# Performance work log

Measured on AMD Instinct MI355X. Metric: run time of the kernel, lower is better.

## Reference

```python
import jax, jax.numpy as jnp
import numpy as np

B, T_TREES, LEAVES = 1024, 34, 16
E = 128            # entity = logic = theorem embedding size
N_NF, N_LF = 4, 3  # binary numerical / logic function experts
V_ENT, V_TH = 2000, 32
GT_MAX, ENT_MAX, TH_MAX = 8, 16, 8


def setup_inputs() -> dict:
    key = jax.random.key(0)
    ks = jax.random.split(key, 24)
    s2e = 1.0 / np.sqrt(2 * E)
    s4e = 1.0 / np.sqrt(4 * E)
    se = 1.0 / np.sqrt(E)
    inp = {
        'leaf_idx': jax.random.randint(ks[0], (B, T_TREES, LEAVES), 0, V_ENT),
        'nf_ids':   jax.random.randint(ks[1], (B, T_TREES, 15), 0, N_NF),
        'lf_ids':   jax.random.randint(ks[2], (B, GT_MAX + 1), 0, N_LF),
        'th_idx':   jax.random.randint(ks[3], (B, TH_MAX), 0, V_TH),
        'ent_emb':  jax.random.normal(ks[4], (V_ENT, E)) * 0.02,
        'th_emb':   jax.random.normal(ks[5], (V_TH, E)) * 0.02,
        # nf two2one expert MLPs: Linear(2E,2E) -> ReLU -> Linear(2E,E)
        'nf_W1': jax.random.normal(ks[6], (N_NF, 2 * E, 2 * E)) * s2e,
        'nf_b1': jnp.zeros((N_NF, 2 * E)),
        'nf_W2': jax.random.normal(ks[7], (N_NF, 2 * E, E)) * s2e,
        'nf_b2': jnp.zeros((N_NF, E)),
        # lf two2one expert MLPs: Linear(2E,4E) -> ReLU -> Linear(4E,E)
        'lf_W1': jax.random.normal(ks[8], (N_LF, 2 * E, 4 * E)) * s2e,
        'lf_b1': jnp.zeros((N_LF, 4 * E)),
        'lf_W2': jax.random.normal(ks[9], (N_LF, 4 * E, E)) * s4e,
        'lf_b2': jnp.zeros((N_LF, E)),
        # higher attention linears: logic_size -> {entity,entity,theorem} size
        'he_W': jax.random.normal(ks[10], (E, E)) * se, 'he_b': jnp.zeros((E,)),
        'hg_W': jax.random.normal(ks[11], (E, E)) * se, 'hg_b': jnp.zeros((E,)),
        'ht_W': jax.random.normal(ks[12], (E, E)) * se, 'ht_b': jnp.zeros((E,)),
    }
    return inp


def _expert_mlp(x, ids, W1, b1, W2, b2):
    # x: [..., Din], ids: [...] selecting among K experts; masked sum over K (small fixed loop)
    out = jnp.zeros(x.shape[:-1] + (W2.shape[-1],), x.dtype)
    for k in range(W1.shape[0]):
        h = jax.nn.relu(x @ W1[k] + b1[k]) @ W2[k] + b2[k]
        out = out + jnp.where((ids == k)[..., None], h, 0.0)
    return out


def _attend(keys, q):
    # keys: [B, N, D], q: [B, D] -> attentive context [B, D]
    a = jax.nn.softmax(jnp.einsum('bnd,bd->bn', keys, q), axis=-1)
    return jnp.einsum('bn,bnd->bd', a, keys)


def _forward(leaf_idx, nf_ids, lf_ids, th_idx, ent_emb, th_emb,
             nf_W1, nf_b1, nf_W2, nf_b2, lf_W1, lf_b1, lf_W2, lf_b2,
             he_W, he_b, hg_W, hg_b, ht_W, ht_b):
    # leaf entity embedding lookup: [B, 34, 16, E]
    cur = ent_emb[leaf_idx]
    # recursive tree reduction over 4 levels of binary nf MLPs (batched over all nodes)
    off = 0
    for lvl in range(4):
        n = LEAVES >> (lvl + 1)  # nodes at this level: 8,4,2,1
        x = cur.reshape(cur.shape[0], T_TREES, n, 2 * E)  # concat(left,right)
        ids = nf_ids[..., off:off + n]
        off += n
        cur = _expert_mlp(x, ids, nf_W1, nf_b1, nf_W2, nf_b2)
    roots = cur[..., 0, :]                       # [B, 34, E]
    ent = roots[:, :ENT_MAX]                     # [B, 16, E] standalone entities
    pairs = roots[:, ENT_MAX:].reshape(roots.shape[0], GT_MAX + 1, 2 * E)
    stmt = _expert_mlp(pairs, lf_ids, lf_W1, lf_b1, lf_W2, lf_b2)  # [B, 9, E]
    gt = stmt[:, :GT_MAX]                        # [B, 8, E] ground truths
    obj = stmt[:, GT_MAX]                        # [B, E]    objective
    th = th_emb[th_idx]                          # [B, 8, E] theorems
    ent_ctx = _attend(ent, obj @ he_W + he_b)
    gt_ctx = _attend(gt, obj @ hg_W + hg_b)
    th_ctx = _attend(th, obj @ ht_W + ht_b)
    # higher attentive state: 2*L + E + T = 512
    return jnp.concatenate([obj, gt_ctx, ent_ctx, th_ctx], axis=-1)


def reference(leaf_idx, nf_ids, lf_ids, th_idx, ent_emb, th_emb,
              nf_W1, nf_b1, nf_W2, nf_b2, lf_W1, lf_b1, lf_W2, lf_b2,
              he_W, he_b, hg_W, hg_b, ht_W, ht_b):
    return _forward(leaf_idx, nf_ids, lf_ids, th_idx, ent_emb, th_emb,
                    nf_W1, nf_b1, nf_W2, nf_b2, lf_W1, lf_b1, lf_W2, lf_b2,
                    he_W, he_b, hg_W, hg_b, ht_W, ht_b)
```

## Files before the change

### kernel.cpp

```cpp
#include <hip/hip_runtime.h>
#include <math.h>


typedef unsigned short u16;
typedef unsigned int   u32;
typedef unsigned long long u64;
typedef __attribute__((ext_vector_type(8))) short v8s;
typedef __attribute__((ext_vector_type(4))) float f32x4;

__device__ __forceinline__ float b2f(u16 u) { return __uint_as_float(((u32)u) << 16); }
__device__ __forceinline__ u16 f2b(float f) {
  f = (f == f) ? f : 0.f;
  u32 x = __float_as_uint(f);
  u32 r = x + 0x7fffu + ((x >> 16) & 1u);
  return (u16)(r >> 16);
}

__device__ __forceinline__ void g2lds16(const void* g, void* l) {
  __builtin_amdgcn_global_load_lds(
      (const __attribute__((address_space(1))) void*)g,
      (__attribute__((address_space(3))) void*)l, 16, 0, 0);
}

#define NTREE 34816
#define RLEAF 9216


__global__ __launch_bounds__(256) void perm_hist_k(
    const int* __restrict__ nf, int* __restrict__ bh,
    const int CB, const int bt0, const int nb)
{
  const int gid = blockIdx.x * 256 + threadIdx.x;
  int id = -1, lr = 0, cofs = 12, ioff = 14, shift = 0;
  if (gid < 8 * CB)       { lr = gid;          cofs = 0;  ioff = 0;  shift = 3; }
  else if (gid < 12 * CB) { lr = gid - 8*CB;   cofs = 4;  ioff = 8;  shift = 2; }
  else if (gid < 14 * CB) { lr = gid - 12*CB;  cofs = 8;  ioff = 12; shift = 1; }
  else if (gid < 15 * CB) { lr = gid - 14*CB;          }
  if (gid < 15 * CB) {
    int bt = bt0 + (lr >> shift);
    int n  = lr & ((1 << shift) - 1);
    id = nf[bt * 15 + ioff + n];
  }
  __shared__ int lcnt[16];
  if (threadIdx.x < 16) lcnt[threadIdx.x] = 0;
  __syncthreads();
  const int lane = threadIdx.x & 63;
  #pragma unroll
  for (int e = 0; e < 4; ++e) {
    u64 m = __ballot(id == e);
    if (m && lane == __builtin_ctzll(m))
      atomicAdd(&lcnt[cofs + e], (int)__popcll(m));
  }
  __syncthreads();
  if (threadIdx.x < 16)
    bh[threadIdx.x * nb + blockIdx.x] = lcnt[threadIdx.x];
}

__global__ __launch_bounds__(1024) void perm_scan_k(
    int* __restrict__ bh, int* __restrict__ cnt, const int nb)
{
  const int s = threadIdx.x >> 6;
  const int lane = threadIdx.x & 63;
  int carry = 0;
  for (int b0 = 0; b0 < nb; b0 += 64) {
    const int b = b0 + lane;
    int v = (b < nb) ? bh[s * nb + b] : 0;
    int x = v;
    #pragma unroll
    for (int d = 1; d < 64; d <<= 1) {
      int y = __shfl_up(x, d);
      if (lane >= d) x += y;
    }
    if (b < nb) bh[s * nb + b] = carry + x - v;
    carry += __shfl(x, 63);
  }
  if (lane == 0) cnt[s] = carry;
}

__global__ __launch_bounds__(256) void perm_scatter_k(
    const int* __restrict__ nf, const int* __restrict__ bh,
    int* __restrict__ perm, const int CB, const int bt0, const int nb)
{
  const int gid = blockIdx.x * 256 + threadIdx.x;
  int id = -1, lr = 0, rows = CB, cofs = 12, pofs = 56 * CB, ioff = 14, shift = 0;
  if (gid < 8 * CB)       { lr = gid;          rows = 8*CB; cofs = 0;  pofs = 0;      ioff = 0;  shift = 3; }
  else if (gid < 12 * CB) { lr = gid - 8*CB;   rows = 4*CB; cofs = 4;  pofs = 32*CB;  ioff = 8;  shift = 2; }
  else if (gid < 14 * CB) { lr = gid - 12*CB;  rows = 2*CB; cofs = 8;  pofs = 48*CB;  ioff = 12; shift = 1; }
  else if (gid < 15 * CB) { lr = gid - 14*CB;                 }
  if (gid < 15 * CB) {
    int bt = bt0 + (lr >> shift);
    int n  = lr & ((1 << shift) - 1);
    id = nf[bt * 15 + ioff + n];
  }
  __shared__ int wc[4][16];
  const int w = threadIdx.x >> 6, lane = threadIdx.x & 63;
  if (lane < 16) wc[w][lane] = 0;
  __syncthreads();
  u64 msave[4];
  #pragma unroll
  for (int e = 0; e < 4; ++e) {
    u64 m = __ballot(id == e);
    msave[e] = m;
    if (m && lane == __builtin_ctzll(m))
      wc[w][cofs + e] = (int)__popcll(m);
  }
  __syncthreads();
  #pragma unroll
  for (int e = 0; e < 4; ++e) {
    if (id == e) {
      const int slot = cofs + e;
      int base = bh[slot * nb + blockIdx.x];
      #pragma unroll
      for (int w2 = 0; w2 < 3; ++w2)
        if (w2 < w) base += wc[w2][slot];
      perm[pofs + e * rows + base +
           (int)__popcll(msave[e] & ((1ull << lane) - 1ull))] = lr;
    }
  }
}

__global__ __launch_bounds__(256) void leaf_perm_k(
    const int* __restrict__ lf, int* __restrict__ cnt, int* __restrict__ perm)
{
  const int gid = blockIdx.x * 256 + threadIdx.x;
  const int id = lf[gid];
  const int lane = threadIdx.x & 63;
  for (int e = 0; e < 3; ++e) {
    u64 m = __ballot(id == e);
    if (!m) continue;
    int leader = __builtin_ctzll(m);
    int bp = 0;
    if (lane == leader) bp = atomicAdd(&cnt[e], (int)__popcll(m));
    bp = __shfl(bp, leader);
    if (id == e)
      perm[e * RLEAF + bp + (int)__popcll(m & ((1ull << lane) - 1ull))] = gid;
  }
}

__global__ __launch_bounds__(256) void transpose_k(
    const float* __restrict__ s0, const float* __restrict__ s1,
    const float* __restrict__ s2, const float* __restrict__ s3,
    const float* __restrict__ s4,
    u16* __restrict__ d0, u16* __restrict__ d1, u16* __restrict__ d2,
    u16* __restrict__ d3, u16* __restrict__ d4)
{
  __shared__ float tile[16][17];
  const int t = threadIdx.x;
  const int idx0 = blockIdx.x * 256;
  if (idx0 < 983040) {
    const float* s; u16* d; int tb, estr, O, kt, mt, e;
    int tloc0;
    if (idx0 < 262144)      { s = s0; d = d0; tb = 0;      estr = 65536;  O = 256; }
    else if (idx0 < 393216) { s = s1; d = d1; tb = 262144; estr = 32768;  O = 128; }
    else if (idx0 < 786432) { s = s2; d = d2; tb = 393216; estr = 131072; O = 512; }
    else                    { s = s3; d = d3; tb = 786432; estr = 65536;  O = 128; }
    tloc0 = idx0 - tb;
    const int blk = tloc0 >> 9;
    const int hb  = (tloc0 >> 8) & 1;
    if (idx0 < 262144)      { kt = blk & 7;  mt = (blk >> 3) & 15; e = blk >> 7; }
    else if (idx0 < 393216) { kt = blk & 7;  mt = (blk >> 3) & 7;  e = blk >> 6; }
    else if (idx0 < 786432) { kt = blk & 7;  mt = (blk >> 3) & 31; e = blk >> 8; }
    else                    { kt = blk & 15; mt = (blk >> 4) & 7;  e = blk >> 7; }
    const int o0 = mt * 16;
    const int k0 = kt * 32 + hb * 16;
    tile[t >> 4][t & 15] = s[(size_t)e * estr + (size_t)(k0 + (t >> 4)) * O + o0 + (t & 15)];
    __syncthreads();
    d[tloc0 + t] = f2b(tile[((t >> 7) << 3) + (t & 7)][(t >> 3) & 15]);
  } else {
    int tl = idx0 + t - 983040;
    d4[tl] = f2b(s4[tl]);
  }
}

template<int HID, int NEXP, int MODE, int MR>
__global__ __launch_bounds__(256, 2) void mlp_k(
    const u16* __restrict__ src, const int* __restrict__ lidx,
    const u16* __restrict__ emb,
    const int* __restrict__ perm, const int* __restrict__ cnt,
    const int rows, const int bt0,
    const u16* __restrict__ W1f, const float* __restrict__ b1,
    const u16* __restrict__ W2f, const float* __restrict__ b2,
    u16* __restrict__ dst)
{
  constexpr int NT  = MR / 16;
  constexpr int MT1 = HID / 64;
  constexpr int K2  = HID / 32;
  constexpr int PD1 = (MT1 <= 4) ? 2 : 1;
  constexpr int NB1 = PD1 + 1;
  constexpr int XB  = MR * 512;
  constexpr int HB  = MR * HID * 2;
  constexpr int UB  = XB > HB ? XB : HB;
  __shared__ __align__(16) char uni[UB];
  __shared__ int rid[MR], soff[2 * MR];
  u16* const xs = (u16*)uni;
  u16* const hs = (u16*)uni;

  int bin = -1, tile = 0, cb = 0;
  {
    int rem = blockIdx.x;
    #pragma unroll
    for (int e = 0; e < NEXP; ++e) {
      int ce = cnt[e];
      int tt = (ce + MR - 1) / MR;
      if (bin < 0) {
        if (rem < tt) { bin = e; tile = rem; cb = ce; }
        else rem -= tt;
      }
    }
  }
  if (bin < 0) return;
  const int rbase = tile * MR;
  const int tid = threadIdx.x;
  const int w  = tid >> 6;
  const int lane = tid & 63;
  const int lm = lane & 15;
  const int lq = lane >> 4;

  const u16* const W1b = W1f + ((size_t)(bin * (HID / 16) + w * MT1) << 12) + lane * 8;
  const u16* const W2b = W2f + ((size_t)((bin * 8 + w * 2) * K2) << 9) + lane * 8;

  v8s afb[NB1][MT1];
  #pragma unroll
  for (int d = 0; d < PD1; ++d)
    #pragma unroll
    for (int m = 0; m < MT1; ++m)
      afb[d][m] = *(const v8s*)(W1b + (size_t)(m * 8 + d) * 512);

  if (tid < MR) {
    int rl = rbase + tid;
    int rlc = rl < cb ? rl : (cb - 1);
    rlc = rlc < 0 ? 0 : rlc;
    int rc = perm[(size_t)bin * rows + rlc];
    rc = rc < 0 ? 0 : (rc >= rows ? rows - 1 : rc);
    rid[tid] = (rl < cb) ? rc : -1;
    if (MODE == 0) {
      int bt = bt0 + (rc >> 3), node = rc & 7;
      int ia = lidx[bt * 16 + node * 2];
      int ib = lidx[bt * 16 + node * 2 + 1];
      ia = ia < 0 ? 0 : (ia > 1999 ? 1999 : ia);
      ib = ib < 0 ? 0 : (ib > 1999 ? 1999 : ib);
      soff[2 * tid]     = ia * 256;
      soff[2 * tid + 1] = ib * 256;
    } else {
      int base;
      if (MODE == 1) base = rc * 512;
      else { int bq = rc / 9, g = rc - bq * 9; base = (bq * 34 + 16 + 2 * g) * 256; }
      soff[2 * tid]     = base;
      soff[2 * tid + 1] = base + 256;
    }
  }
  __syncthreads();

  const char* const sb = (MODE == 0) ? (const char*)emb : (const char*)src;
  #pragma unroll
  for (int i = 0; i < MR / 8; ++i) {
    int d = i * 256 + tid;
    int r = d >> 5, c32d = d & 31;
    int cS = c32d ^ ((r & 7) << 1);
    const char* ga = sb + (size_t)(u32)soff[2 * r + (cS >> 4)] + (cS & 15) * 16;
    char* la = uni + ((size_t)(i * 256 + (tid & 192)) << 4);
    g2lds16(ga, la);
  }
  __syncthreads();

  int rdn[NT];
  #pragma unroll
  for (int n = 0; n < NT; ++n) rdn[n] = rid[n * 16 + lm];

  f32x4 acc[MT1][NT];
  #pragma unroll
  for (int m = 0; m < MT1; ++m)
    #pragma unroll
    for (int n = 0; n < NT; ++n)
      acc[m][n] = f32x4{0.f, 0.f, 0.f, 0.f};

  v8s bfr2[2][NT];
  #pragma unroll
  for (int n = 0; n < NT; ++n) {
    int r = n * 16 + lm;
    int cs = lq ^ ((lm & 7) << 1);
    bfr2[0][n] = *(const v8s*)(xs + r * 256 + cs * 8);
  }
  #pragma unroll
  for (int k = 0; k < 8; ++k) {
    const int cur = k % NB1;
    if (k + PD1 < 8) {
      const int nx = (k + PD1) % NB1;
      #pragma unroll
      for (int m = 0; m < MT1; ++m)
        afb[nx][m] = *(const v8s*)(W1b + (size_t)(m * 8 + k + PD1) * 512);
    }
    const int cb_ = k & 1;
    if (k < 7) {
      #pragma unroll
      for (int n = 0; n < NT; ++n) {
        int r = n * 16 + lm;
        int cs = ((k + 1) * 4 + lq) ^ ((lm & 7) << 1);
        bfr2[cb_ ^ 1][n] = *(const v8s*)(xs + r * 256 + cs * 8);
      }
    }
    __builtin_amdgcn_s_setprio(1);
    #pragma unroll
    for (int m = 0; m < MT1; ++m)
      #pragma unroll
      for (int n = 0; n < NT; ++n)
        acc[m][n] = __builtin_amdgcn_mfma_f32_16x16x32_bf16(afb[cur][m], bfr2[cb_][n], acc[m][n], 0, 0, 0);
    __builtin_amdgcn_s_setprio(0);
  }

  v8s afb2[3][2];
  #pragma unroll
  for (int m = 0; m < 2; ++m)
    afb2[0][m] = *(const v8s*)(W2b + (size_t)(m * K2) * 512);
  #pragma unroll
  for (int m = 0; m < 2; ++m)
    afb2[1][m] = *(const v8s*)(W2b + (size_t)(m * K2 + 1) * 512);

  __syncthreads();

  const float* b1b = b1 + bin * HID;
  #pragma unroll
  for (int m = 0; m < MT1; ++m) {
    const int f = (w * MT1 + m) * 16 + lq * 4;
    float bb0 = b1b[f], bb1 = b1b[f + 1], bb2 = b1b[f + 2], bb3 = b1b[f + 3];
    #pragma unroll
    for (int n = 0; n < NT; ++n) {
      union { u16 h[4]; uint2 v; } pk;
      f32x4 a = acc[m][n];
      pk.h[0] = f2b(fmaxf(a.x + bb0, 0.f));
      pk.h[1] = f2b(fmaxf(a.y + bb1, 0.f));
      pk.h[2] = f2b(fmaxf(a.z + bb2, 0.f));
      pk.h[3] = f2b(fmaxf(a.w + bb3, 0.f));
      int r = n * 16 + lm;
      int cs = (f >> 3) ^ ((lm & 7) << 1);
      *(uint2*)(uni + (size_t)r * (HID * 2) + (cs << 4) + (f & 7) * 2) = pk.v;
    }
  }
  __syncthreads();

  f32x4 acc2[2][NT];
  #pragma unroll
  for (int m = 0; m < 2; ++m)
    #pragma unroll
    for (int n = 0; n < NT; ++n)
      acc2[m][n] = f32x4{0.f, 0.f, 0.f, 0.f};

  #pragma unroll
  for (int n = 0; n < NT; ++n) {
    int r = n * 16 + lm;
    int cs = lq ^ ((lm & 7) << 1);
    bfr2[0][n] = *(const v8s*)(hs + (size_t)r * HID + cs * 8);
  }
  #pragma unroll
  for (int k = 0; k < K2; ++k) {
    const int cur = k % 3;
    if (k < K2 - 2) {
      const int nx2 = (k + 2) % 3;
      #pragma unroll
      for (int m = 0; m < 2; ++m)
        afb2[nx2][m] = *(const v8s*)(W2b + (size_t)(m * K2 + k + 2) * 512);
    }
    const int cb_ = k & 1;
    if (k < K2 - 1) {
      #pragma unroll
      for (int n = 0; n < NT; ++n) {
        int r = n * 16 + lm;
        int cs = ((k + 1) * 4 + lq) ^ ((lm & 7) << 1);
        bfr2[cb_ ^ 1][n] = *(const v8s*)(hs + (size_t)r * HID + cs * 8);
      }
    }
    __builtin_amdgcn_s_setprio(1);
    #pragma unroll
    for (int m = 0; m < 2; ++m)
      #pragma unroll
      for (int n = 0; n < NT; ++n)
        acc2[m][n] = __builtin_amdgcn_mfma_f32_16x16x32_bf16(afb2[cur][m], bfr2[cb_][n], acc2[m][n], 0, 0, 0);
    __builtin_amdgcn_s_setprio(0);
  }

  __syncthreads();
  const float* b2b = b2 + bin * 128;
  #pragma unroll
  for (int m = 0; m < 2; ++m) {
    const int f = (w * 2 + m) * 16 + lq * 4;
    float bb0 = b2b[f], bb1 = b2b[f + 1], bb2 = b2b[f + 2], bb3 = b2b[f + 3];
    #pragma unroll
    for (int n = 0; n < NT; ++n) {
      union { u16 h[4]; uint2 v; } pk;
      f32x4 a = acc2[m][n];
      pk.h[0] = f2b(a.x + bb0);
      pk.h[1] = f2b(a.y + bb1);
      pk.h[2] = f2b(a.z + bb2);
      pk.h[3] = f2b(a.w + bb3);
      int r = n * 16 + lm;
      int c = (w * 2 + m) * 2 + (lq >> 1);
      int cs = c ^ ((lm & 7) << 1);
      *(uint2*)(uni + r * 256 + cs * 16 + (lq & 1) * 8) = pk.v;
    }
  }
  __syncthreads();
  #pragma unroll
  for (int i = 0; i < MR / 16; ++i) {
    int cg = i * 256 + tid;
    int r = cg >> 4, sub = cg & 15;
    int rg = rid[r];
    if (rg >= 0) {
      uint4 v = *(const uint4*)(uni + r * 256 + ((sub ^ ((r & 7) << 1)) << 4));
      *(uint4*)((char*)dst + (size_t)rg * 256 + sub * 16) = v;
    }
  }
}

__global__ __launch_bounds__(128) void attn_k(
    const u16* __restrict__ stmt, const u16* __restrict__ roots,
    const float* __restrict__ themb, const int* __restrict__ thidx,
    const float* __restrict__ wHe, const float* __restrict__ bHe,
    const float* __restrict__ wHg, const float* __restrict__ bHg,
    const float* __restrict__ wHt, const float* __restrict__ bHt,
    float* __restrict__ out)
{
  const int b = blockIdx.x, t = threadIdx.x;
  __shared__ float obj_s[128], q_s[128], keys_s[16 * 132], a_s[16];

  const float obj = b2f(stmt[((size_t)b * 9 + 8) * 128 + t]);
  obj_s[t] = obj;
  out[(size_t)b * 512 + t] = obj;
  __syncthreads();

  for (int a = 0; a < 3; ++a) {
    int cntk;
    const float *Wt, *bv;
    if (a == 0) {
      cntk = 8; Wt = wHg; bv = bHg;
      for (int j = 0; j < 8; ++j)
        keys_s[j * 132 + t] = b2f(stmt[((size_t)b * 9 + j) * 128 + t]);
    } else if (a == 1) {
      cntk = 16; Wt = wHe; bv = bHe;
      for (int j = 0; j < 16; ++j)
        keys_s[j * 132 + t] = b2f(roots[((size_t)b * 34 + j) * 128 + t]);
    } else {
      cntk = 8; Wt = wHt; bv = bHt;
      for (int j = 0; j < 8; ++j) {
        int ti = thidx[b * 8 + j] & 31;
        keys_s[j * 132 + t] = themb[(size_t)ti * 128 + t];
      }
    }
    float qa = bv[t];
    for (int k = 0; k < 128; ++k) qa += obj_s[k] * Wt[k * 128 + t];
    q_s[t] = (qa == qa) ? qa : 0.f;
    __syncthreads();
    {
      int j = t >> 3, s = t & 7;
      if (j < cntk) {
        float sc = 0.f;
        #pragma unroll
        for (int k = 0; k < 16; ++k)
          sc += keys_s[j * 132 + s * 16 + k] * q_s[s * 16 + k];
        sc += __shfl_xor(sc, 1);
        sc += __shfl_xor(sc, 2);
        sc += __shfl_xor(sc, 4);
        if (s == 0) a_s[j] = (sc == sc) ? sc : 0.f;
      }
    }
    __syncthreads();
    if (t < 16) {
      float v = (t < cntk) ? a_s[t] : -3.0e38f;
      float mx = v;
      #pragma unroll
      for (int d = 1; d < 16; d <<= 1) mx = fmaxf(mx, __shfl_xor(mx, d));
      float e = (t < cntk) ? expf(v - mx) : 0.f;
      float sm = e;
      #pragma unroll
      for (int d = 1; d < 16; d <<= 1) sm += __shfl_xor(sm, d);
      if (t < cntk) a_s[t] = e / sm;
    }
    __syncthreads();
    float c = 0.f;
    for (int j = 0; j < cntk; ++j) c += a_s[j] * keys_s[j * 132 + t];
    out[(size_t)b * 512 + 128 * (a + 1) + t] = c;
    __syncthreads();
  }
}

extern "C" void kernel_launch(void* const* d_in, const int* in_sizes, int n_in,
                              void* d_out, int out_size, void* d_ws, size_t ws_size,
                              hipStream_t stream)
{
  const int*   leaf_idx = (const int*)d_in[0];
  const int*   nf_ids   = (const int*)d_in[1];
  const int*   lf_ids   = (const int*)d_in[2];
  const int*   th_idx   = (const int*)d_in[3];
  const float* ent_emb  = (const float*)d_in[4];
  const float* th_emb   = (const float*)d_in[5];
  const float* nf_W1 = (const float*)d_in[6];
  const float* nf_b1 = (const float*)d_in[7];
  const float* nf_W2 = (const float*)d_in[8];
  const float* nf_b2 = (const float*)d_in[9];
  const float* lf_W1 = (const float*)d_in[10];
  const float* lf_b1 = (const float*)d_in[11];
  const float* lf_W2 = (const float*)d_in[12];
  const float* lf_b2 = (const float*)d_in[13];
  const float* he_W = (const float*)d_in[14];
  const float* he_b = (const float*)d_in[15];
  const float* hg_W = (const float*)d_in[16];
  const float* hg_b = (const float*)d_in[17];
  const float* ht_W = (const float*)d_in[18];
  const float* ht_b = (const float*)d_in[19];

  int CB = NTREE;
  while (CB > 544 && 14500000ull + (unsigned long long)CB * 3320ull > (unsigned long long)ws_size)
    CB >>= 1;
  const int nch = NTREE / CB;
  const int NB = (15 * CB + 255) / 256;

  char* ws = (char*)d_ws;
  size_t off = 0;
  auto take = [&](size_t bytes) -> char* {
    char* p = ws + off;
    off = (off + bytes + 255) & ~(size_t)255;
    return p;
  };
  int* cnt      = (int*)take(8192);
  int* leafperm = (int*)take((size_t)3 * RLEAF * 4);
  int* chperm   = (int*)take((size_t)60 * CB * 4);
  int* bh       = (int*)take((size_t)16 * NB * 4);
  u16* wN1  = (u16*)take((size_t)4 * 256 * 256 * 2);
  u16* wN2  = (u16*)take((size_t)4 * 128 * 256 * 2);
  u16* wL1  = (u16*)take((size_t)3 * 512 * 256 * 2);
  u16* wL2  = (u16*)take((size_t)3 * 128 * 512 * 2);
  u16* embB = (u16*)take((size_t)2000 * 128 * 2);
  u16* bufA  = (u16*)take((size_t)CB * 8 * 128 * 2);
  u16* bufB  = (u16*)take((size_t)CB * 4 * 128 * 2);
  u16* roots = (u16*)take((size_t)NTREE * 128 * 2);
  u16* stmt  = (u16*)take((size_t)RLEAF * 128 * 2);

  int* leafcnt = cnt + nch * 16;

  hipMemsetAsync(cnt, 0, (size_t)(nch * 16 + 8) * 4, stream);
  transpose_k<<<4840, 256, 0, stream>>>(nf_W1, nf_W2, lf_W1, lf_W2, ent_emb,
                                        wN1, wN2, wL1, wL2, embB);
  leaf_perm_k<<<36, 256, 0, stream>>>(lf_ids, leafcnt, leafperm);

  for (int c = 0; c < nch; ++c) {
    const int bt0 = c * CB;
    int* ccnt = cnt + c * 16;
    perm_hist_k<<<NB, 256, 0, stream>>>(nf_ids, bh, CB, bt0, NB);
    perm_scan_k<<<1, 1024, 0, stream>>>(bh, ccnt, NB);
    perm_scatter_k<<<NB, 256, 0, stream>>>(nf_ids, bh, chperm, CB, bt0, NB);
    mlp_k<256, 4, 0, 96><<<(8 * CB + 95) / 96 + 4, 256, 0, stream>>>(
        nullptr, leaf_idx, embB, chperm, ccnt, 8 * CB, bt0,
        wN1, nf_b1, wN2, nf_b2, bufA);
    mlp_k<256, 4, 1, 96><<<(4 * CB + 95) / 96 + 4, 256, 0, stream>>>(
        bufA, nullptr, nullptr, chperm + 32 * CB, ccnt + 4, 4 * CB, 0,
        wN1, nf_b1, wN2, nf_b2, bufB);
    mlp_k<256, 4, 1, 64><<<(2 * CB + 63) / 64 + 4, 256, 0, stream>>>(
        bufB, nullptr, nullptr, chperm + 48 * CB, ccnt + 8, 2 * CB, 0,
        wN1, nf_b1, wN2, nf_b2, bufA);
    mlp_k<256, 4, 1, 64><<<(CB + 63) / 64 + 4, 256, 0, stream>>>(
        bufA, nullptr, nullptr, chperm + 56 * CB, ccnt + 12, CB, 0,
        wN1, nf_b1, wN2, nf_b2, roots + (size_t)bt0 * 128);
  }

  mlp_k<512, 3, 2, 32><<<RLEAF / 32 + 3, 256, 0, stream>>>(
      roots, nullptr, nullptr, leafperm, leafcnt, RLEAF, 0,
      wL1, lf_b1, wL2, lf_b2, stmt);

  attn_k<<<1024, 128, 0, stream>>>(stmt, roots, th_emb, th_idx,
                                   he_W, he_b, hg_W, hg_b, ht_W, ht_b,
                                   (float*)d_out);
}
```

Baseline: 292.7 us.

## Merge setup kernels and hoist per-chunk histograms into one launch

Folds the weight transpose/bf16 conversion, the leaf expert permutation and the per-chunk numeric-function histograms into a single setup kernel. The per-chunk scans then run as one multi-block launch, so fewer small kernels are launched and the chunk loop now only holds the scatter and MLP kernels. The histogram buffer is sized per chunk and the workspace budget estimate is raised a little to match. Separately, the attention query projection is unrolled with four partial accumulators to shorten the dependent FMA chain.

```diff
diff --git a/kernel.cpp b/kernel.cpp
--- a/kernel.cpp
+++ b/kernel.cpp
@@ -25,56 +25,113 @@
 #define NTREE 34816
 #define RLEAF 9216
 
-
-__global__ __launch_bounds__(256) void perm_hist_k(
+__global__ __launch_bounds__(256) void setup_k(
+    const float* __restrict__ s0, const float* __restrict__ s1,
+    const float* __restrict__ s2, const float* __restrict__ s3,
+    const float* __restrict__ s4,
+    u16* __restrict__ d0, u16* __restrict__ d1, u16* __restrict__ d2,
+    u16* __restrict__ d3, u16* __restrict__ d4,
+    const int* __restrict__ lf, int* __restrict__ leafcnt, int* __restrict__ leafperm,
     const int* __restrict__ nf, int* __restrict__ bh,
-    const int CB, const int bt0, const int nb)
+    const int CB, const int NB)
 {
-  const int gid = blockIdx.x * 256 + threadIdx.x;
-  int id = -1, lr = 0, cofs = 12, ioff = 14, shift = 0;
-  if (gid < 8 * CB)       { lr = gid;          cofs = 0;  ioff = 0;  shift = 3; }
-  else if (gid < 12 * CB) { lr = gid - 8*CB;   cofs = 4;  ioff = 8;  shift = 2; }
-  else if (gid < 14 * CB) { lr = gid - 12*CB;  cofs = 8;  ioff = 12; shift = 1; }
-  else if (gid < 15 * CB) { lr = gid - 14*CB;          }
-  if (gid < 15 * CB) {
-    int bt = bt0 + (lr >> shift);
-    int n  = lr & ((1 << shift) - 1);
-    id = nf[bt * 15 + ioff + n];
-  }
+  __shared__ float tile[16][17];
   __shared__ int lcnt[16];
-  if (threadIdx.x < 16) lcnt[threadIdx.x] = 0;
-  __syncthreads();
-  const int lane = threadIdx.x & 63;
-  #pragma unroll
-  for (int e = 0; e < 4; ++e) {
-    u64 m = __ballot(id == e);
-    if (m && lane == __builtin_ctzll(m))
-      atomicAdd(&lcnt[cofs + e], (int)__popcll(m));
-  }
-  __syncthreads();
-  if (threadIdx.x < 16)
-    bh[threadIdx.x * nb + blockIdx.x] = lcnt[threadIdx.x];
+  const int t = threadIdx.x;
+  const int bid = blockIdx.x;
+
+  if (bid < 4840) {
+    const int idx0 = bid * 256;
+    if (idx0 < 983040) {
+      const float* s; u16* d; int tb, estr, O, kt, mt, e;
+      int tloc0;
+      if (idx0 < 262144)      { s = s0; d = d0; tb = 0;      estr = 65536;  O = 256; }
+      else if (idx0 < 393216) { s = s1; d = d1; tb = 262144; estr = 32768;  O = 128; }
+      else if (idx0 < 786432) { s = s2; d = d2; tb = 393216; estr = 131072; O = 512; }
+      else                    { s = s3; d = d3; tb = 786432; estr = 65536;  O = 128; }
+      tloc0 = idx0 - tb;
+      const int blk = tloc0 >> 9;
+      const int hb  = (tloc0 >> 8) & 1;
+      if (idx0 < 262144)      { kt = blk & 7;  mt = (blk >> 3) & 15; e = blk >> 7; }
+      else if (idx0 < 393216) { kt = blk & 7;  mt = (blk >> 3) & 7;  e = blk >> 6; }
+      else if (idx0 < 786432) { kt = blk & 7;  mt = (blk >> 3) & 31; e = blk >> 8; }
+      else                    { kt = blk & 15; mt = (blk >> 4) & 7;  e = blk >> 7; }
+      const int o0 = mt * 16;
+      const int k0 = kt * 32 + hb * 16;
+      tile[t >> 4][t & 15] = s[(size_t)e * estr + (size_t)(k0 + (t >> 4)) * O + o0 + (t & 15)];
+      __syncthreads();
+      d[tloc0 + t] = f2b(tile[((t >> 7) << 3) + (t & 7)][(t >> 3) & 15]);
+    } else {
+      int tl = idx0 + t - 983040;
+      d4[tl] = f2b(s4[tl]);
+    }
+  } else if (bid < 4876) {
+    const int gid = (bid - 4840) * 256 + t;
+    const int id = lf[gid];
+    const int lane = t & 63;
+    for (int e = 0; e < 3; ++e) {
+      u64 m = __ballot(id == e);
+      if (!m) continue;
+      int leader = __builtin_ctzll(m);
+      int bp = 0;
+      if (lane == leader) bp = atomicAdd(&leafcnt[e], (int)__popcll(m));
+      bp = __shfl(bp, leader);
+      if (id == e)
+        leafperm[e * RLEAF + bp + (int)__popcll(m & ((1ull << lane) - 1ull))] = gid;
+    }
+  } else {
+    const int hb2 = bid - 4876;
+    const int c = hb2 / NB, b = hb2 - c * NB;
+    const int bt0 = c * CB;
+    int* bhc = bh + (size_t)c * 16 * NB;
+    const int gid = b * 256 + t;
+    int id = -1, lr = 0, cofs = 12, ioff = 14, shift = 0;
+    if (gid < 8 * CB)       { lr = gid;          cofs = 0;  ioff = 0;  shift = 3; }
+    else if (gid < 12 * CB) { lr = gid - 8*CB;   cofs = 4;  ioff = 8;  shift = 2; }
+    else if (gid < 14 * CB) { lr = gid - 12*CB;  cofs = 8;  ioff = 12; shift = 1; }
+    else if (gid < 15 * CB) { lr = gid - 14*CB;  }
+    if (gid < 15 * CB) {
+      int bt = bt0 + (lr >> shift);
+      int n  = lr & ((1 << shift) - 1);
+      id = nf[bt * 15 + ioff + n];
+    }
+    if (t < 16) lcnt[t] = 0;
+    __syncthreads();
+    const int lane = t & 63;
+    #pragma unroll
+    for (int e = 0; e < 4; ++e) {
+      u64 m = __ballot(id == e);
+      if (m && lane == __builtin_ctzll(m))
+        atomicAdd(&lcnt[cofs + e], (int)__popcll(m));
+    }
+    __syncthreads();
+    if (t < 16)
+      bhc[t * NB + b] = lcnt[t];
+  }
 }
 
 __global__ __launch_bounds__(1024) void perm_scan_k(
     int* __restrict__ bh, int* __restrict__ cnt, const int nb)
 {
+  const int c = blockIdx.x;
+  int* bhc = bh + (size_t)c * 16 * nb;
+  int* cntc = cnt + c * 16;
   const int s = threadIdx.x >> 6;
   const int lane = threadIdx.x & 63;
   int carry = 0;
   for (int b0 = 0; b0 < nb; b0 += 64) {
     const int b = b0 + lane;
-    int v = (b < nb) ? bh[s * nb + b] : 0;
+    int v = (b < nb) ? bhc[s * nb + b] : 0;
     int x = v;
     #pragma unroll
     for (int d = 1; d < 64; d <<= 1) {
       int y = __shfl_up(x, d);
       if (lane >= d) x += y;
     }
-    if (b < nb) bh[s * nb + b] = carry + x - v;
+    if (b < nb) bhc[s * nb + b] = carry + x - v;
     carry += __shfl(x, 63);
   }
-  if (lane == 0) cnt[s] = carry;
+  if (lane == 0) cntc[s] = carry;
 }
 
 __global__ __launch_bounds__(256) void perm_scatter_k(
@@ -116,59 +173,6 @@
       perm[pofs + e * rows + base +
            (int)__popcll(msave[e] & ((1ull << lane) - 1ull))] = lr;
     }
-  }
-}
-
-__global__ __launch_bounds__(256) void leaf_perm_k(
-    const int* __restrict__ lf, int* __restrict__ cnt, int* __restrict__ perm)
-{
-  const int gid = blockIdx.x * 256 + threadIdx.x;
-  const int id = lf[gid];
-  const int lane = threadIdx.x & 63;
-  for (int e = 0; e < 3; ++e) {
-    u64 m = __ballot(id == e);
-    if (!m) continue;
-    int leader = __builtin_ctzll(m);
-    int bp = 0;
-    if (lane == leader) bp = atomicAdd(&cnt[e], (int)__popcll(m));
-    bp = __shfl(bp, leader);
-    if (id == e)
-      perm[e * RLEAF + bp + (int)__popcll(m & ((1ull << lane) - 1ull))] = gid;
-  }
-}
-
-__global__ __launch_bounds__(256) void transpose_k(
-    const float* __restrict__ s0, const float* __restrict__ s1,
-    const float* __restrict__ s2, const float* __restrict__ s3,
-    const float* __restrict__ s4,
-    u16* __restrict__ d0, u16* __restrict__ d1, u16* __restrict__ d2,
-    u16* __restrict__ d3, u16* __restrict__ d4)
-{
-  __shared__ float tile[16][17];
-  const int t = threadIdx.x;
-  const int idx0 = blockIdx.x * 256;
-  if (idx0 < 983040) {
-    const float* s; u16* d; int tb, estr, O, kt, mt, e;
-    int tloc0;
-    if (idx0 < 262144)      { s = s0; d = d0; tb = 0;      estr = 65536;  O = 256; }
-    else if (idx0 < 393216) { s = s1; d = d1; tb = 262144; estr = 32768;  O = 128; }
-    else if (idx0 < 786432) { s = s2; d = d2; tb = 393216; estr = 131072; O = 512; }
-    else                    { s = s3; d = d3; tb = 786432; estr = 65536;  O = 128; }
-    tloc0 = idx0 - tb;
-    const int blk = tloc0 >> 9;
-    const int hb  = (tloc0 >> 8) & 1;
-    if (idx0 < 262144)      { kt = blk & 7;  mt = (blk >> 3) & 15; e = blk >> 7; }
-    else if (idx0 < 393216) { kt = blk & 7;  mt = (blk >> 3) & 7;  e = blk >> 6; }
-    else if (idx0 < 786432) { kt = blk & 7;  mt = (blk >> 3) & 31; e = blk >> 8; }
-    else                    { kt = blk & 15; mt = (blk >> 4) & 7;  e = blk >> 7; }
-    const int o0 = mt * 16;
-    const int k0 = kt * 32 + hb * 16;
-    tile[t >> 4][t & 15] = s[(size_t)e * estr + (size_t)(k0 + (t >> 4)) * O + o0 + (t & 15)];
-    __syncthreads();
-    d[tloc0 + t] = f2b(tile[((t >> 7) << 3) + (t & 7)][(t >> 3) & 15]);
-  } else {
-    int tl = idx0 + t - 983040;
-    d4[tl] = f2b(s4[tl]);
   }
 }
 
@@ -445,8 +449,15 @@
         keys_s[j * 132 + t] = themb[(size_t)ti * 128 + t];
       }
     }
-    float qa = bv[t];
-    for (int k = 0; k < 128; ++k) qa += obj_s[k] * Wt[k * 128 + t];
+    float q0 = 0.f, q1 = 0.f, q2 = 0.f, q3 = 0.f;
+    #pragma unroll 4
+    for (int k = 0; k < 128; k += 4) {
+      q0 += obj_s[k]     * Wt[(k)     * 128 + t];
+      q1 += obj_s[k + 1] * Wt[(k + 1) * 128 + t];
+      q2 += obj_s[k + 2] * Wt[(k + 2) * 128 + t];
+      q3 += obj_s[k + 3] * Wt[(k + 3) * 128 + t];
+    }
+    float qa = bv[t] + ((q0 + q1) + (q2 + q3));
     q_s[t] = (qa == qa) ? qa : 0.f;
     __syncthreads();
     {
@@ -508,7 +519,7 @@
   const float* ht_b = (const float*)d_in[19];
 
   int CB = NTREE;
-  while (CB > 544 && 14500000ull + (unsigned long long)CB * 3320ull > (unsigned long long)ws_size)
+  while (CB > 544 && 14700000ull + (unsigned long long)CB * 3320ull > (unsigned long long)ws_size)
     CB >>= 1;
   const int nch = NTREE / CB;
   const int NB = (15 * CB + 255) / 256;
@@ -523,7 +534,7 @@
   int* cnt      = (int*)take(8192);
   int* leafperm = (int*)take((size_t)3 * RLEAF * 4);
   int* chperm   = (int*)take((size_t)60 * CB * 4);
-  int* bh       = (int*)take((size_t)16 * NB * 4);
+  int* bh       = (int*)take((size_t)nch * 16 * NB * 4);
   u16* wN1  = (u16*)take((size_t)4 * 256 * 256 * 2);
   u16* wN2  = (u16*)take((size_t)4 * 128 * 256 * 2);
   u16* wL1  = (u16*)take((size_t)3 * 512 * 256 * 2);
@@ -536,17 +547,17 @@
 
   int* leafcnt = cnt + nch * 16;
 
-  hipMemsetAsync(cnt, 0, (size_t)(nch * 16 + 8) * 4, stream);
-  transpose_k<<<4840, 256, 0, stream>>>(nf_W1, nf_W2, lf_W1, lf_W2, ent_emb,
-                                        wN1, wN2, wL1, wL2, embB);
-  leaf_perm_k<<<36, 256, 0, stream>>>(lf_ids, leafcnt, leafperm);
+  hipMemsetAsync(leafcnt, 0, 8 * 4, stream);
+  setup_k<<<4876 + nch * NB, 256, 0, stream>>>(
+      nf_W1, nf_W2, lf_W1, lf_W2, ent_emb, wN1, wN2, wL1, wL2, embB,
+      lf_ids, leafcnt, leafperm, nf_ids, bh, CB, NB);
+  perm_scan_k<<<nch, 1024, 0, stream>>>(bh, cnt, NB);
 
   for (int c = 0; c < nch; ++c) {
     const int bt0 = c * CB;
     int* ccnt = cnt + c * 16;
-    perm_hist_k<<<NB, 256, 0, stream>>>(nf_ids, bh, CB, bt0, NB);
-    perm_scan_k<<<1, 1024, 0, stream>>>(bh, ccnt, NB);
-    perm_scatter_k<<<NB, 256, 0, stream>>>(nf_ids, bh, chperm, CB, bt0, NB);
+    perm_scatter_k<<<NB, 256, 0, stream>>>(nf_ids, bh + (size_t)c * 16 * NB,
+                                           chperm, CB, bt0, NB);
     mlp_k<256, 4, 0, 96><<<(8 * CB + 95) / 96 + 4, 256, 0, stream>>>(
         nullptr, leaf_idx, embB, chperm, ccnt, 8 * CB, bt0,
         wN1, nf_b1, wN2, nf_b2, bufA);
```

New measurement: 296.8 us. No clear change (+1.4%).
